# Kernel optimization log

Measured on AMD Instinct MI355X. Metric: run time of the kernel, lower is better.

The kernel has to match this reference:

```python
import jax, jax.numpy as jnp
import numpy as np

D, DFF, H, K = 512, 2048, 8, 31
DK = D // H
EPS = 1e-5


def _ln(x, g, b):
    m = jnp.mean(x, axis=-1, keepdims=True)
    v = jnp.mean((x - m) ** 2, axis=-1, keepdims=True)
    return (x - m) * jax.lax.rsqrt(v + EPS) * g + b


def _ffn(x, w1, b1, w2, b2):
    return jax.nn.silu(x @ w1 + b1) @ w2 + b2


def _rel_shift(x):
    # x: (B, H, T, P) with P = 2T-1
    b, h, q, p = x.shape
    x = jnp.pad(x, ((0, 0), (0, 0), (0, 0), (1, 0)))
    x = x.reshape(b, h, p + 1, q)[:, :, 1:, :]
    return x.reshape(b, h, q, p)


def setup_inputs() -> dict:
    key = jax.random.key(0)
    ks = jax.random.split(key, 32)
    r = lambda i, shape: 0.02 * jax.random.normal(ks[i], shape, dtype=jnp.float32)
    B, T = 4, 1024
    inp = {
        'x': jax.random.normal(ks[0], (B, T, D), dtype=jnp.float32),
        'pos_emb': jax.random.normal(ks[1], (1, 2 * T - 1, D), dtype=jnp.float32),
        # LayerNorms (5)
        'ln1_g': jnp.ones((D,)), 'ln1_b': jnp.zeros((D,)),
        'ln2_g': jnp.ones((D,)), 'ln2_b': jnp.zeros((D,)),
        'ln3_g': jnp.ones((D,)), 'ln3_b': jnp.zeros((D,)),
        'ln4_g': jnp.ones((D,)), 'ln4_b': jnp.zeros((D,)),
        'ln5_g': jnp.ones((D,)), 'ln5_b': jnp.zeros((D,)),
        # FFN1
        'ff1_w1': r(2, (D, DFF)), 'ff1_b1': jnp.zeros((DFF,)),
        'ff1_w2': r(3, (DFF, D)), 'ff1_b2': jnp.zeros((D,)),
        # Attention
        'wq': r(4, (D, D)), 'bq': jnp.zeros((D,)),
        'wk': r(5, (D, D)), 'bk': jnp.zeros((D,)),
        'wv': r(6, (D, D)), 'bv': jnp.zeros((D,)),
        'wp': r(7, (D, D)),
        'wo': r(8, (D, D)), 'bo': jnp.zeros((D,)),
        'pos_u': r(9, (H, DK)), 'pos_v': r(10, (H, DK)),
        # Conv module
        'pw1_w': r(11, (2 * D, D)), 'pw1_b': jnp.zeros((2 * D,)),
        'dw_w': r(12, (D, 1, K)), 'dw_b': jnp.zeros((D,)),
        'bn_g': jnp.ones((D,)), 'bn_b': jnp.zeros((D,)),
        'pw2_w': r(13, (D, D)), 'pw2_b': jnp.zeros((D,)),
        # FFN2
        'ff2_w1': r(14, (D, DFF)), 'ff2_b1': jnp.zeros((DFF,)),
        'ff2_w2': r(15, (DFF, D)), 'ff2_b2': jnp.zeros((D,)),
    }
    return inp


def _attn(x, pos_emb, wq, bq, wk, bk, wv, bv, wp, wo, bo, pos_u, pos_v):
    B, T, _ = x.shape
    q = (x @ wq + bq).reshape(B, T, H, DK).transpose(0, 2, 1, 3)
    k = (x @ wk + bk).reshape(B, T, H, DK).transpose(0, 2, 1, 3)
    v = (x @ wv + bv).reshape(B, T, H, DK).transpose(0, 2, 1, 3)
    P = pos_emb.shape[1]
    p = (pos_emb[0] @ wp).reshape(P, H, DK)  # (P, H, DK)
    ac = jnp.einsum('bhqd,bhkd->bhqk', q + pos_u[:, None, :], k)
    bd = jnp.einsum('bhqd,phd->bhqp', q + pos_v[:, None, :], p)
    bd = _rel_shift(bd)[:, :, :, :T]
    scores = (ac + bd) * (DK ** -0.5)
    attn = jax.nn.softmax(scores, axis=-1)
    out = jnp.einsum('bhqk,bhkd->bhqd', attn, v)
    out = out.transpose(0, 2, 1, 3).reshape(B, T, D)
    return out @ wo + bo


def _conv(x, pw1_w, pw1_b, dw_w, dw_b, bn_g, bn_b, pw2_w, pw2_b):
    y = x.transpose(0, 2, 1)  # (B, D, T)
    y = jnp.einsum('od,bdt->bot', pw1_w, y) + pw1_b[:, None]
    a, g = jnp.split(y, 2, axis=1)
    y = a * jax.nn.sigmoid(g)  # GLU
    pad = (K - 1) // 2
    y = jax.lax.conv_general_dilated(
        y, dw_w, (1,), [(pad, pad)],
        dimension_numbers=('NCW', 'OIW', 'NCW'), feature_group_count=D)
    y = y + dw_b[:, None]
    m = jnp.mean(y, axis=(0, 2), keepdims=True)
    var = jnp.mean((y - m) ** 2, axis=(0, 2), keepdims=True)
    y = (y - m) * jax.lax.rsqrt(var + EPS) * bn_g[:, None] + bn_b[:, None]
    y = jax.nn.silu(y)
    y = jnp.einsum('od,bdt->bot', pw2_w, y) + pw2_b[:, None]
    return y.transpose(0, 2, 1)


def reference(x, pos_emb,
              ln1_g, ln1_b, ff1_w1, ff1_b1, ff1_w2, ff1_b2,
              ln2_g, ln2_b, wq, bq, wk, bk, wv, bv, wp, wo, bo, pos_u, pos_v,
              ln3_g, ln3_b, pw1_w, pw1_b, dw_w, dw_b, bn_g, bn_b, pw2_w, pw2_b,
              ln4_g, ln4_b, ff2_w1, ff2_b1, ff2_w2, ff2_b2,
              ln5_g, ln5_b):
    h = x + 0.5 * _ffn(_ln(x, ln1_g, ln1_b), ff1_w1, ff1_b1, ff1_w2, ff1_b2)
    h = h + _attn(_ln(h, ln2_g, ln2_b), pos_emb, wq, bq, wk, bk, wv, bv, wp, wo, bo, pos_u, pos_v)
    h = h + _conv(_ln(h, ln3_g, ln3_b), pw1_w, pw1_b, dw_w, dw_b, bn_g, bn_b, pw2_w, pw2_b)
    h = h + 0.5 * _ffn(_ln(h, ln4_g, ln4_b), ff2_w1, ff2_b1, ff2_w2, ff2_b2)
    return _ln(h, ln5_g, ln5_b)
```

## Files before the change

kernel.cpp:

```cpp
#include <hip/hip_runtime.h>
#include <math.h>

#define TT   1024
#define BBZ  4
#define DD   512
#define DFF_ 2048
#define HH   8
#define DKK  64
#define NTOK 4096
#define EPSF 1e-5f
#define MB   1048576
#define QSCALE 0.18033688011112042f
#define M0OFF  24.0f

typedef unsigned short u16;
typedef __attribute__((ext_vector_type(8))) short s8v;
typedef __attribute__((ext_vector_type(4))) float f32x4;
typedef __attribute__((ext_vector_type(4))) unsigned short us4;
typedef __attribute__((ext_vector_type(8))) unsigned short us8;

__device__ __forceinline__ float b2f(u16 v){
    union { unsigned int u; float f; } x; x.u = ((unsigned int)v) << 16; return x.f;
}
__device__ __forceinline__ u16 f2b(float f){
    union { float f; unsigned int u; } x; x.f = f;
    unsigned int r = x.u + 0x7fffu + ((x.u >> 16) & 1u);
    return (u16)(r >> 16);
}
__device__ __forceinline__ float sigmoidf_(float x){ return 1.0f/(1.0f+__expf(-x)); }

__device__ __forceinline__ void gld16(const u16* g, u16* l){
    __builtin_amdgcn_global_load_lds(
        (const __attribute__((address_space(1))) unsigned int*)g,
        (__attribute__((address_space(3))) unsigned int*)l, 16, 0, 0);
}

template<int OMODE>
__global__ __launch_bounds__(256) void bgemm128(
    const u16* __restrict__ A, int lda,
    const u16* __restrict__ B, int ldb,
    void* __restrict__ Cv, int ldc, int K,
    const float* __restrict__ bias, int act)
{
    int n0 = blockIdx.x * 128;
    int m0 = blockIdx.y * 128;

    __shared__ u16 As[128*64];
    __shared__ u16 Bs[128*64];

    int t = threadIdx.x;
    int w = t >> 6, l = t & 63;
    int lrow = l >> 3, lslot = l & 7;
    int kswz = (lslot ^ lrow) * 8;
    int wm = w >> 1, wn = w & 1;
    int lr = l & 15, lk = l >> 4;

    f32x4 acc[4][4] = {};

    for (int k0 = 0; k0 < K; k0 += 64){
        #pragma unroll
        for (int it = 0; it < 4; ++it){
            int rb = it*32 + w*8;
            gld16(A + (size_t)(m0 + rb + lrow)*lda + k0 + kswz, &As[rb*64]);
            gld16(B + (size_t)(n0 + rb + lrow)*ldb + k0 + kswz, &Bs[rb*64]);
        }
        __syncthreads();

        s8v af[2][4], bf[2][4];
        #pragma unroll
        for (int kh = 0; kh < 2; ++kh){
            int sl = (kh*4 + lk) ^ (lr & 7);
            #pragma unroll
            for (int mi = 0; mi < 4; ++mi)
                af[kh][mi] = *(const s8v*)&As[(wm*64 + mi*16 + lr)*64 + sl*8];
            #pragma unroll
            for (int ni = 0; ni < 4; ++ni)
                bf[kh][ni] = *(const s8v*)&Bs[(wn*64 + ni*16 + lr)*64 + sl*8];
        }
        #pragma unroll
        for (int kh = 0; kh < 2; ++kh)
            #pragma unroll
            for (int mi = 0; mi < 4; ++mi)
                #pragma unroll
                for (int ni = 0; ni < 4; ++ni)
                    acc[mi][ni] = __builtin_amdgcn_mfma_f32_16x16x32_bf16(
                        af[kh][mi], bf[kh][ni], acc[mi][ni], 0, 0, 0);
        __syncthreads();
    }

    #pragma unroll
    for (int mi = 0; mi < 4; ++mi){
        #pragma unroll
        for (int ni = 0; ni < 4; ++ni){
            int gn = n0 + wn*64 + ni*16 + lr;
            float bval = bias ? bias[gn] : 0.0f;
            #pragma unroll
            for (int r = 0; r < 4; ++r){
                int gm = m0 + wm*64 + mi*16 + lk*4 + r;
                float vv = acc[mi][ni][r] + bval;
                if (act) vv = vv * sigmoidf_(vv);
                if (OMODE == 1){
                    ((u16*)Cv)[(size_t)gm*ldc + gn] = f2b(vv);
                } else {
                    u16* base = (u16*)Cv;
                    size_t idx = (gn < 512)
                        ? ((size_t)gm*512 + gn)*2
                        : ((size_t)gm*512 + (gn-512))*2 + 1;
                    base[idx] = f2b(vv);
                }
            }
        }
    }
}

__global__ __launch_bounds__(256) void qkvp_gemm(
    const u16* __restrict__ xn, const u16* __restrict__ wqT,
    const u16* __restrict__ posb, const u16* __restrict__ wpT,
    u16* __restrict__ qkvbase, u16* __restrict__ pproj,
    const float* __restrict__ bqkv,
    const float* __restrict__ posu, const float* __restrict__ posv)
{
    bool isP = (blockIdx.x >= 12);
    if (isP && blockIdx.y >= 16) return;
    const u16* A = isP ? posb : xn;
    const u16* B = isP ? wpT : wqT;
    int n0 = isP ? (blockIdx.x - 12)*128 : blockIdx.x*128;
    int m0 = blockIdx.y * 128;

    __shared__ u16 As[128*64];
    __shared__ u16 Bs[128*64];

    int t = threadIdx.x;
    int w = t >> 6, l = t & 63;
    int lrow = l >> 3, lslot = l & 7;
    int kswz = (lslot ^ lrow) * 8;
    int wm = w >> 1, wn = w & 1;
    int lr = l & 15, lk = l >> 4;

    f32x4 acc[4][4] = {};

    for (int k0 = 0; k0 < 512; k0 += 64){
        #pragma unroll
        for (int it = 0; it < 4; ++it){
            int rb = it*32 + w*8;
            gld16(A + (size_t)(m0 + rb + lrow)*512 + k0 + kswz, &As[rb*64]);
            gld16(B + (size_t)(n0 + rb + lrow)*512 + k0 + kswz, &Bs[rb*64]);
        }
        __syncthreads();

        s8v af[2][4], bf[2][4];
        #pragma unroll
        for (int kh = 0; kh < 2; ++kh){
            int sl = (kh*4 + lk) ^ (lr & 7);
            #pragma unroll
            for (int mi = 0; mi < 4; ++mi)
                af[kh][mi] = *(const s8v*)&As[(wm*64 + mi*16 + lr)*64 + sl*8];
            #pragma unroll
            for (int ni = 0; ni < 4; ++ni)
                bf[kh][ni] = *(const s8v*)&Bs[(wn*64 + ni*16 + lr)*64 + sl*8];
        }
        #pragma unroll
        for (int kh = 0; kh < 2; ++kh)
            #pragma unroll
            for (int mi = 0; mi < 4; ++mi)
                #pragma unroll
                for (int ni = 0; ni < 4; ++ni)
                    acc[mi][ni] = __builtin_amdgcn_mfma_f32_16x16x32_bf16(
                        af[kh][mi], bf[kh][ni], acc[mi][ni], 0, 0, 0);
        __syncthreads();
    }

    #pragma unroll
    for (int mi = 0; mi < 4; ++mi){
        #pragma unroll
        for (int ni = 0; ni < 4; ++ni){
            int gn = n0 + wn*64 + ni*16 + lr;
            float bval = isP ? 0.0f : bqkv[gn];
            #pragma unroll
            for (int r = 0; r < 4; ++r){
                int gm = m0 + wm*64 + mi*16 + lk*4 + r;
                float vv = acc[mi][ni][r] + bval;
                if (isP){
                    pproj[(size_t)gm*512 + gn] = f2b(vv);
                } else {
                    u16* base = qkvbase;
                    if (gn < 512){
                        size_t idx = (size_t)gm*512 + gn;
                        base[idx]              = f2b((vv + posu[gn])*QSCALE);
                        base[idx + (2u<<20)]   = f2b((vv + posv[gn])*QSCALE);
                    } else if (gn < 1024){
                        base[(4u<<20) + (size_t)gm*512 + (gn-512)] = f2b(vv);
                    } else {
                        int gnp = gn - 1024;
                        int bb = gm >> 10, tt2 = gm & 1023;
                        size_t idx = (((size_t)(bb*8 + (gnp>>6)))*64 + (gnp&63))*1024 + tt2;
                        base[(6u<<20) + idx] = f2b(vv);
                    }
                }
            }
        }
    }
}

__global__ __launch_bounds__(256) void bgemm64(
    const u16* __restrict__ A, int lda,
    const u16* __restrict__ B, int ldb,
    u16* __restrict__ C, int ldc, int K,
    const float* __restrict__ bias, float alpha,
    const u16* __restrict__ resid)
{
    int n0 = blockIdx.x * 64;
    int m0 = blockIdx.y * 64;

    __shared__ u16 As[64*64];
    __shared__ u16 Bs[64*64];

    int t = threadIdx.x;
    int w = t >> 6, l = t & 63;
    int lrow = l >> 3, lslot = l & 7;
    int kswz = (lslot ^ lrow) * 8;
    int wm = w >> 1, wn = w & 1;
    int lr = l & 15, lk = l >> 4;

    f32x4 acc[2][2] = {};

    for (int k0 = 0; k0 < K; k0 += 64){
        #pragma unroll
        for (int it = 0; it < 2; ++it){
            int rb = it*32 + w*8;
            gld16(A + (size_t)(m0 + rb + lrow)*lda + k0 + kswz, &As[rb*64]);
            gld16(B + (size_t)(n0 + rb + lrow)*ldb + k0 + kswz, &Bs[rb*64]);
        }
        __syncthreads();

        s8v af[2][2], bf[2][2];
        #pragma unroll
        for (int kh = 0; kh < 2; ++kh){
            int sl = (kh*4 + lk) ^ (lr & 7);
            #pragma unroll
            for (int mi = 0; mi < 2; ++mi)
                af[kh][mi] = *(const s8v*)&As[(wm*32 + mi*16 + lr)*64 + sl*8];
            #pragma unroll
            for (int ni = 0; ni < 2; ++ni)
                bf[kh][ni] = *(const s8v*)&Bs[(wn*32 + ni*16 + lr)*64 + sl*8];
        }
        #pragma unroll
        for (int kh = 0; kh < 2; ++kh)
            #pragma unroll
            for (int mi = 0; mi < 2; ++mi)
                #pragma unroll
                for (int ni = 0; ni < 2; ++ni)
                    acc[mi][ni] = __builtin_amdgcn_mfma_f32_16x16x32_bf16(
                        af[kh][mi], bf[kh][ni], acc[mi][ni], 0, 0, 0);
        __syncthreads();
    }

    #pragma unroll
    for (int mi = 0; mi < 2; ++mi){
        #pragma unroll
        for (int ni = 0; ni < 2; ++ni){
            int gn = n0 + wn*32 + ni*16 + lr;
            float bval = bias ? bias[gn] : 0.0f;
            #pragma unroll
            for (int r = 0; r < 4; ++r){
                int gm = m0 + wm*32 + mi*16 + lk*4 + r;
                float vv = (acc[mi][ni][r] + bval) * alpha;
                if (resid) vv += b2f(resid[(size_t)gm*ldc + gn]);
                C[(size_t)gm*ldc + gn] = f2b(vv);
            }
        }
    }
}

__global__ __launch_bounds__(256) void bgemm64k(
    const u16* __restrict__ A, int lda,
    const u16* __restrict__ B, int ldb,
    u16* __restrict__ C, int ldc, int K,
    const float* __restrict__ bias, float alpha,
    const float* __restrict__ residF, const u16* __restrict__ residB)
{
    int n0 = blockIdx.x * 64;
    int m0 = blockIdx.y * 64;

    __shared__ u16 As[64*128];
    __shared__ u16 Bs[64*128];

    int t = threadIdx.x;
    int w = t >> 6, l = t & 63;
    int r4 = l >> 4;
    int s16 = l & 15;
    int kswz = (s16 ^ (w*4 + r4)) * 8;
    int wm = w >> 1, wn = w & 1;
    int lr = l & 15, lk = l >> 4;

    f32x4 acc[2][2] = {};

    for (int k0 = 0; k0 < K; k0 += 128){
        #pragma unroll
        for (int cb = 0; cb < 4; ++cb){
            int rowu = cb*16 + w*4;
            gld16(A + (size_t)(m0 + rowu + r4)*lda + k0 + kswz, &As[rowu*128]);
            gld16(B + (size_t)(n0 + rowu + r4)*ldb + k0 + kswz, &Bs[rowu*128]);
        }
        __syncthreads();

        #pragma unroll
        for (int kh = 0; kh < 4; ++kh){
            int sl = ((kh*4 + lk) ^ lr) * 8;
            s8v af[2], bf[2];
            #pragma unroll
            for (int mi = 0; mi < 2; ++mi)
                af[mi] = *(const s8v*)&As[(wm*32 + mi*16 + lr)*128 + sl];
            #pragma unroll
            for (int ni = 0; ni < 2; ++ni)
                bf[ni] = *(const s8v*)&Bs[(wn*32 + ni*16 + lr)*128 + sl];
            #pragma unroll
            for (int mi = 0; mi < 2; ++mi)
                #pragma unroll
                for (int ni = 0; ni < 2; ++ni)
                    acc[mi][ni] = __builtin_amdgcn_mfma_f32_16x16x32_bf16(
                        af[mi], bf[ni], acc[mi][ni], 0, 0, 0);
        }
        __syncthreads();
    }

    #pragma unroll
    for (int mi = 0; mi < 2; ++mi){
        #pragma unroll
        for (int ni = 0; ni < 2; ++ni){
            int gn = n0 + wn*32 + ni*16 + lr;
            float bval = bias ? bias[gn] : 0.0f;
            #pragma unroll
            for (int r = 0; r < 4; ++r){
                int gm = m0 + wm*32 + mi*16 + lk*4 + r;
                float vv = (acc[mi][ni][r] + bval) * alpha;
                size_t idx = (size_t)gm*ldc + gn;
                if (residF) vv += residF[idx];
                if (residB) vv += b2f(residB[idx]);
                C[idx] = f2b(vv);
            }
        }
    }
}

__global__ __launch_bounds__(256) void attn_fused(
    const u16* __restrict__ qub, const u16* __restrict__ qvb,
    const u16* __restrict__ kb,  const u16* __restrict__ vt,
    const u16* __restrict__ pp,  u16* __restrict__ out)
{
    int z = blockIdx.y;
    int b = z >> 3, hh = z & 7;
    int i0 = blockIdx.x * 64;

    __shared__ u16 Kb2[2][64*64];
    __shared__ u16 Vb2[2][64*64];
    __shared__ u16 Pring[3][64*64];
    __shared__ u16 PT[64*64];
    __shared__ float Bandd[4][1024];

    int t = threadIdx.x;
    int w = t >> 6, l = t & 63;
    int lrow = l >> 3, lslot = l & 7;
    int kswz = (lslot ^ lrow) * 8;
    int lr = l & 15, lk = l >> 4;

    #pragma unroll
    for (int it = 0; it < 2; ++it){
        int rb = it*32 + w*8;
        gld16(qub + (size_t)(b*TT + i0 + rb + lrow)*DD + hh*64 + kswz, &PT[rb*64]);
        gld16(qvb + (size_t)(b*TT + i0 + rb + lrow)*DD + hh*64 + kswz,
              (u16*)&Bandd[0][0] + rb*64);
    }
    __syncthreads();
    s8v af_u[2], af_v[2];
    #pragma unroll
    for (int kh = 0; kh < 2; ++kh){
        int sl = (kh*4 + lk) ^ (lr & 7);
        af_u[kh] = *(const s8v*)&PT[(w*16 + lr)*64 + sl*8];
        af_v[kh] = *(const s8v*)((const u16*)&Bandd[0][0] + (w*16 + lr)*64 + sl*8);
    }
    #pragma unroll
    for (int it = 0; it < 2; ++it){
        int rb = it*32 + w*8;
        gld16(kb + (size_t)(b*TT +        rb + lrow)*DD + hh*64 + kswz, &Kb2[0][rb*64]);
        gld16(vt + ((size_t)z*64 + rb + lrow)*TT +                kswz, &Vb2[0][rb*64]);
        gld16(pp + (size_t)(960  - i0 +   rb + lrow)*DD + hh*64 + kswz, &Pring[0][rb*64]);
        gld16(pp + (size_t)(1024 - i0 +   rb + lrow)*DD + hh*64 + kswz, &Pring[1][rb*64]);
    }

    f32x4 o_[4] = {};
    float Lp[4] = {0.f, 0.f, 0.f, 0.f};

    int s0 = 0, s1 = 1, s2 = 2;

    for (int jt = 0; jt < 16; ++jt){
        int cur = jt & 1;
        __syncthreads();

        if (jt < 15){
            #pragma unroll
            for (int it = 0; it < 2; ++it){
                int rb = it*32 + w*8;
                gld16(kb + (size_t)(b*TT + (jt+1)*64 + rb + lrow)*DD + hh*64 + kswz,
                      &Kb2[cur^1][rb*64]);
                gld16(vt + ((size_t)z*64 + rb + lrow)*TT + (jt+1)*64 + kswz,
                      &Vb2[cur^1][rb*64]);
                gld16(pp + (size_t)(960 + (jt+2)*64 - i0 + rb + lrow)*DD + hh*64 + kswz,
                      &Pring[s2][rb*64]);
            }
        }

        f32x4 sac[4] = {};
        f32x4 g[5] = {};
        __builtin_amdgcn_s_setprio(1);
        #pragma unroll
        for (int kh = 0; kh < 2; ++kh){
            int sl = (kh*4 + lk) ^ (lr & 7);
            #pragma unroll
            for (int n = 0; n < 4; ++n){
                s8v bK = *(const s8v*)&Kb2[cur][(n*16 + lr)*64 + sl*8];
                sac[n] = __builtin_amdgcn_mfma_f32_16x16x32_bf16(af_u[kh], bK, sac[n], 0,0,0);
            }
            #pragma unroll
            for (int n = 0; n < 5; ++n){
                int nn = (3 - w) + n;
                const u16* pc = (nn & 4) ? &Pring[s1][0] : &Pring[s0][0];
                s8v bP = *(const s8v*)&pc[(((nn&3)*16) + lr)*64 + sl*8];
                g[n] = __builtin_amdgcn_mfma_f32_16x16x32_bf16(af_v[kh], bP, g[n], 0,0,0);
            }
        }
        __builtin_amdgcn_s_setprio(0);

        #pragma unroll
        for (int n = 0; n < 4; ++n){
            int c = (3 - w + n)*16 + lr;
            int d = (c - 63) & 63;
            int rho = (d >> 2) & 3;
            f32x4 vv;
            if (n == 0){
                #pragma unroll
                for (int r = 0; r < 4; ++r){
                    int iia = w*16 + lk*4 + r;
                    vv[r] = (iia >= 63 - c) ? g[0][r] : g[4][r];
                }
            } else {
                vv = g[n];
            }
            bool sw1 = rho & 1, sw2 = rho & 2;
            float b0 = sw1 ? vv[1] : vv[0];
            float b1 = sw1 ? vv[0] : vv[1];
            float b2 = sw1 ? vv[3] : vv[2];
            float b3 = sw1 ? vv[2] : vv[3];
            f32x4 vvp;
            vvp[0] = sw2 ? b2 : b0;
            vvp[1] = sw2 ? b3 : b1;
            vvp[2] = sw2 ? b0 : b2;
            vvp[3] = sw2 ? b1 : b3;
            *(f32x4*)&Bandd[w][d*16 + ((lk + d) & 3)*4] = vvp;
        }

        float p_[4][4];
        #pragma unroll
        for (int r = 0; r < 4; ++r){
            int ii_l = lk*4 + r;
            float rs = 0.0f;
            #pragma unroll
            for (int n = 0; n < 4; ++n){
                int jj = n*16 + lr;
                int d  = (jj - 16*w - ii_l) & 63;
                float bd = Bandd[w][d*16 + (((ii_l>>2) + d) & 3)*4
                                         + ((ii_l ^ (d>>2)) & 3)];
                float pv = __builtin_amdgcn_exp2f(sac[n][r] + bd - M0OFF);
                p_[n][r] = pv; rs += pv;
            }
            Lp[r] += rs;
        }

        #pragma unroll
        for (int n = 0; n < 4; ++n)
            #pragma unroll
            for (int r = 0; r < 4; ++r){
                int ii  = w*16 + lk*4 + r;
                int col = n*16 + lr;
                int sl  = (col>>3) ^ (ii&7);
                PT[ii*64 + sl*8 + (col&7)] = f2b(p_[n][r]);
            }

        __builtin_amdgcn_s_setprio(1);
        #pragma unroll
        for (int kh = 0; kh < 2; ++kh){
            int sl = (kh*4 + lk) ^ (lr & 7);
            s8v ap = *(const s8v*)&PT[(w*16 + lr)*64 + sl*8];
            #pragma unroll
            for (int n = 0; n < 4; ++n){
                s8v bV = *(const s8v*)&Vb2[cur][(n*16 + lr)*64 + sl*8];
                o_[n] = __builtin_amdgcn_mfma_f32_16x16x32_bf16(ap, bV, o_[n], 0,0,0);
            }
        }
        __builtin_amdgcn_s_setprio(0);
        int tmp = s0; s0 = s1; s1 = s2; s2 = tmp;
    }

    float Lr[4];
    #pragma unroll
    for (int r = 0; r < 4; ++r){
        float Lv = Lp[r];
        #pragma unroll
        for (int msk = 1; msk < 16; msk <<= 1) Lv += __shfl_xor(Lv, msk);
        Lr[r] = 1.0f / Lv;
    }

    #pragma unroll
    for (int n = 0; n < 4; ++n)
        #pragma unroll
        for (int r = 0; r < 4; ++r){
            int i  = i0 + w*16 + lk*4 + r;
            int dk = n*16 + lr;
            out[(size_t)(b*TT + i)*DD + hh*64 + dk] = f2b(o_[n][r] * Lr[r]);
        }
}

template<int IB, int OB>
__global__ __launch_bounds__(256) void ln_kernel(const void* __restrict__ inp,
    const float* __restrict__ g, const float* __restrict__ b, void* __restrict__ outv)
{
    int w = threadIdx.x >> 6, l = threadIdx.x & 63;
    int row = blockIdx.x*4 + w;
    float v[8];
    if (IB){
        us8 xv = ((const us8*)((const u16*)inp + (size_t)row*DD))[l];
        #pragma unroll
        for (int e=0;e<8;e++) v[e] = b2f(xv[e]);
    } else {
        const float4* xr = (const float4*)((const float*)inp + (size_t)row*DD);
        float4 a = xr[2*l], c = xr[2*l+1];
        v[0]=a.x; v[1]=a.y; v[2]=a.z; v[3]=a.w;
        v[4]=c.x; v[5]=c.y; v[6]=c.z; v[7]=c.w;
    }
    float s = 0.f, q = 0.f;
    #pragma unroll
    for (int e=0;e<8;e++){ s += v[e]; q += v[e]*v[e]; }
    #pragma unroll
    for (int msk = 1; msk < 64; msk <<= 1){
        s += __shfl_xor(s, msk);
        q += __shfl_xor(q, msk);
    }
    float mean = s*(1.0f/DD);
    float var  = q*(1.0f/DD) - mean*mean;
    float rinv = rsqrtf(var+EPSF);
    float4 g0 = ((const float4*)g)[2*l], g1 = ((const float4*)g)[2*l+1];
    float4 b0 = ((const float4*)b)[2*l], b1 = ((const float4*)b)[2*l+1];
    float gv[8] = {g0.x,g0.y,g0.z,g0.w,g1.x,g1.y,g1.z,g1.w};
    float bv[8] = {b0.x,b0.y,b0.z,b0.w,b1.x,b1.y,b1.z,b1.w};
    float y[8];
    #pragma unroll
    for (int e=0;e<8;e++) y[e] = (v[e]-mean)*rinv*gv[e] + bv[e];
    if (OB){
        us8 o;
        #pragma unroll
        for (int e=0;e<8;e++) o[e] = f2b(y[e]);
        ((us8*)((u16*)outv + (size_t)row*DD))[l] = o;
    } else {
        float4 o0 = {y[0],y[1],y[2],y[3]};
        float4 o1 = {y[4],y[5],y[6],y[7]};
        float4* op = (float4*)((float*)outv + (size_t)row*DD);
        op[2*l] = o0; op[2*l+1] = o1;
    }
}

struct Prep9 {
    const float* s[9];
    u16* d[9];
    int R[9], C[9];
    int t0[10];
};

__global__ __launch_bounds__(256) void prep_all(Prep9 P,
    const float* __restrict__ pw1_w, const float* __restrict__ pw2_w,
    const float* __restrict__ pos_emb, const float* __restrict__ dw_w,
    const float* __restrict__ bq, const float* __restrict__ bk,
    const float* __restrict__ bv,
    u16* __restrict__ pw1b, u16* __restrict__ pw2b,
    u16* __restrict__ posb, float* __restrict__ wt, float* __restrict__ bqkv)
{
    __shared__ float tile[32][33];
    int bid = blockIdx.x;
    if (bid < 5376){
        int j = 0;
        #pragma unroll
        for (int e=1; e<9; e++) if (bid >= P.t0[e]) j = e;
        int lb = bid - P.t0[j];
        int nx = P.C[j] >> 5;
        int c0 = (lb % nx) << 5;
        int r0 = (lb / nx) << 5;
        const float* in = P.s[j];
        u16* out = P.d[j];
        int R = P.R[j], C = P.C[j];
        int tx = threadIdx.x & 31, ty = threadIdx.x >> 5;
        #pragma unroll
        for (int i=0;i<4;i++){
            int rr = ty + i*8;
            tile[rr][tx] = in[(size_t)(r0+rr)*C + c0+tx];
        }
        __syncthreads();
        #pragma unroll
        for (int i=0;i<4;i++){
            int cc = ty + i*8;
            out[(size_t)(c0+cc)*R + r0+tx] = f2b(tile[tx][cc]);
        }
        return;
    }
    int i = (bid - 5376)*256 + threadIdx.x;
    if (i < 524288) { pw1b[i] = f2b(pw1_w[i]); return; }
    i -= 524288;
    if (i < 262144) { pw2b[i] = f2b(pw2_w[i]); return; }
    i -= 262144;
    if (i < 1048576) { posb[i] = (i < 2047*512) ? f2b(pos_emb[i]) : (u16)0; return; }
    i -= 1048576;
    if (i < 15872) { int kk = i >> 9, d = i & 511; wt[i] = dw_w[d*31+kk]; return; }
    i -= 15872;
    if (i < 1536) bqkv[i] = (i < 512) ? bq[i] : (i < 1024 ? bk[i-512] : bv[i-1024]);
}

__global__ __launch_bounds__(256) void dwconv_kernel(const unsigned int* __restrict__ t2i,
    const float* __restrict__ wt, const float* __restrict__ bias, u16* __restrict__ z,
    float* __restrict__ stats)
{
    int d  = blockIdx.x*256 + threadIdx.x;
    int c  = blockIdx.y;
    int b  = c >> 7;
    int t0 = (c & 127) << 3;
    const unsigned int* pa = t2i + (size_t)b*TT*512 + d;
    float wv[31];
    #pragma unroll
    for (int kk=0;kk<31;kk++) wv[kk] = wt[kk*512 + d];
    float xv[38];
    #pragma unroll
    for (int e=0;e<38;e++){
        int tp = t0 - 15 + e;
        if (tp >= 0 && tp < TT){
            unsigned int pv = pa[(size_t)tp*512];
            float a  = b2f((u16)(pv & 0xffffu));
            float gg = b2f((u16)(pv >> 16));
            xv[e] = a * sigmoidf_(gg);
        } else xv[e] = 0.0f;
    }
    float bsv = bias[d];
    float s = 0.f, q = 0.f;
    #pragma unroll
    for (int j=0;j<8;j++){
        float sum = bsv;
        #pragma unroll
        for (int kk=0;kk<31;kk++) sum = fmaf(xv[j+kk], wv[kk], sum);
        z[(size_t)(b*TT+t0+j)*DD + d] = f2b(sum);
        s += sum; q += sum*sum;
    }
    atomicAdd(&stats[d],       s);
    atomicAdd(&stats[512 + d], q);
}

__global__ __launch_bounds__(256) void bn_apply_kernel(const u16* __restrict__ z,
    const float* __restrict__ stats, const float* __restrict__ g, const float* __restrict__ b,
    u16* __restrict__ out)
{
    int idx = blockIdx.x*256 + threadIdx.x;
    int c = idx & (DD-1);
    float m   = stats[c]*(1.0f/NTOK);
    float var = stats[DD+c]*(1.0f/NTOK) - m*m;
    float vv  = (b2f(z[idx])-m)*rsqrtf(var+EPSF)*g[c] + b[c];
    out[idx]  = f2b(vv*sigmoidf_(vv));
}

extern "C" void kernel_launch(void* const* d_in, const int* in_sizes, int n_in,
                              void* d_out, int out_size, void* d_ws, size_t ws_size,
                              hipStream_t stream)
{
    const float* x       = (const float*)d_in[0];
    const float* pos_emb = (const float*)d_in[1];
    const float* ln1_g=(const float*)d_in[2],  *ln1_b=(const float*)d_in[3];
    const float* ln2_g=(const float*)d_in[4],  *ln2_b=(const float*)d_in[5];
    const float* ln3_g=(const float*)d_in[6],  *ln3_b=(const float*)d_in[7];
    const float* ln4_g=(const float*)d_in[8],  *ln4_b=(const float*)d_in[9];
    const float* ln5_g=(const float*)d_in[10], *ln5_b=(const float*)d_in[11];
    const float* ff1_w1=(const float*)d_in[12], *ff1_b1=(const float*)d_in[13];
    const float* ff1_w2=(const float*)d_in[14], *ff1_b2=(const float*)d_in[15];
    const float* wq=(const float*)d_in[16], *bq=(const float*)d_in[17];
    const float* wk=(const float*)d_in[18], *bk=(const float*)d_in[19];
    const float* wv=(const float*)d_in[20], *bv=(const float*)d_in[21];
    const float* wp=(const float*)d_in[22];
    const float* wo=(const float*)d_in[23], *bo=(const float*)d_in[24];
    const float* pos_u=(const float*)d_in[25], *pos_v=(const float*)d_in[26];
    const float* pw1_w=(const float*)d_in[27], *pw1_b=(const float*)d_in[28];
    const float* dw_w=(const float*)d_in[29],  *dw_b=(const float*)d_in[30];
    const float* bn_g=(const float*)d_in[31],  *bn_b=(const float*)d_in[32];
    const float* pw2_w=(const float*)d_in[33], *pw2_b=(const float*)d_in[34];
    const float* ff2_w1=(const float*)d_in[35], *ff2_b1=(const float*)d_in[36];
    const float* ff2_w2=(const float*)d_in[37], *ff2_b2=(const float*)d_in[38];

    char* W = (char*)d_ws;
    u16*  h     = (u16*) (W);
    u16*  xn    = (u16*) (W + (size_t) 8*MB);
    u16*  wall  = (u16*) (W + (size_t)12*MB);
    u16*  qub   = (u16*) (W + (size_t)28*MB);
    u16*  qvb   = (u16*) (W + (size_t)32*MB);
    u16*  kb    = (u16*) (W + (size_t)36*MB);
    u16*  vt    = (u16*) (W + (size_t)40*MB);
    u16*  pproj = (u16*) (W + (size_t)44*MB);
    char* big   = W + (size_t)48*MB;
    u16*  ffh   = (u16*)big;
    unsigned int* t2i = (unsigned int*)big;
    u16*  t3u   = (u16*)(big + (size_t)8*MB);
    float* stats= (float*)(W + (size_t)112*MB);
    float* wt   = stats + 4096;
    float* bqkv = wt + 15872;

    u16* ff1w1T = wall;
    u16* ff1w2T = wall + 1048576;
    u16* wqT    = wall + 2097152;
    u16* wkT    = wall + 2359296;
    u16* wvT    = wall + 2621440;
    u16* wpT    = wall + 2883584;
    u16* woT    = wall + 3145728;
    u16* ff2w1T = wall + 3407872;
    u16* ff2w2T = wall + 4456448;
    u16* pw1b   = wall + 5505024;
    u16* pw2b   = wall + 6029312;
    u16* posb   = wall + 6291456;

    dim3 blk(256);

    Prep9 P;
    P.s[0]=ff1_w1; P.d[0]=ff1w1T; P.R[0]=512;  P.C[0]=2048;
    P.s[1]=ff1_w2; P.d[1]=ff1w2T; P.R[1]=2048; P.C[1]=512;
    P.s[2]=wq;     P.d[2]=wqT;    P.R[2]=512;  P.C[2]=512;
    P.s[3]=wk;     P.d[3]=wkT;    P.R[3]=512;  P.C[3]=512;
    P.s[4]=wv;     P.d[4]=wvT;    P.R[4]=512;  P.C[4]=512;
    P.s[5]=wp;     P.d[5]=wpT;    P.R[5]=512;  P.C[5]=512;
    P.s[6]=wo;     P.d[6]=woT;    P.R[6]=512;  P.C[6]=512;
    P.s[7]=ff2_w1; P.d[7]=ff2w1T; P.R[7]=512;  P.C[7]=2048;
    P.s[8]=ff2_w2; P.d[8]=ff2w2T; P.R[8]=2048; P.C[8]=512;
    int tc[9] = {1024,1024,256,256,256,256,256,1024,1024};
    P.t0[0]=0; for (int e=0;e<9;e++) P.t0[e+1]=P.t0[e]+tc[e];
    prep_all<<<dim3(5376+7236), blk, 0, stream>>>(P, pw1_w, pw2_w, pos_emb, dw_w,
                                                  bq, bk, bv,
                                                  pw1b, pw2b, posb, wt, bqkv);

    ln_kernel<0,1><<<dim3(NTOK/4), blk, 0, stream>>>(x, ln1_g, ln1_b, xn);
    bgemm128<1><<<dim3(16,32), blk, 0, stream>>>(xn,512, ff1w1T,512,
        ffh,2048, 512, ff1_b1,1);
    bgemm64k<<<dim3(8,64), blk, 0, stream>>>(ffh,2048, ff1w2T,2048,
        h,512, 2048, ff1_b2,0.5f, x, nullptr);

    ln_kernel<1,1><<<dim3(NTOK/4), blk, 0, stream>>>(h, ln2_g, ln2_b, xn);
    qkvp_gemm<<<dim3(16,32), blk, 0, stream>>>(xn, wqT, posb, wpT,
        qub, pproj, bqkv, pos_u, pos_v);

    attn_fused<<<dim3(16,32), blk, 0, stream>>>(qub, qvb, kb, vt, pproj, xn);

    bgemm64<<<dim3(8,64), blk, 0, stream>>>(xn,512, woT,512,
        h,512, 512, bo,1.f, h);

    ln_kernel<1,1><<<dim3(NTOK/4), blk, 0, stream>>>(h, ln3_g, ln3_b, xn);
    bgemm128<6><<<dim3(8,32), blk, 0, stream>>>(xn,512, pw1b,512,
        t2i,1024, 512, pw1_b,0);
    (void)hipMemsetAsync(stats, 0, 4096, stream);
    dwconv_kernel<<<dim3(2,512), blk, 0, stream>>>(t2i, wt, dw_b, t3u, stats);
    bn_apply_kernel<<<dim3(NTOK*DD/256), blk, 0, stream>>>(t3u, stats, bn_g, bn_b, xn);
    bgemm64<<<dim3(8,64), blk, 0, stream>>>(xn,512, pw2b,512,
        h,512, 512, pw2_b,1.f, h);

    ln_kernel<1,1><<<dim3(NTOK/4), blk, 0, stream>>>(h, ln4_g, ln4_b, xn);
    bgemm128<1><<<dim3(16,32), blk, 0, stream>>>(xn,512, ff2w1T,512,
        ffh,2048, 512, ff2_b1,1);
    bgemm64k<<<dim3(8,64), blk, 0, stream>>>(ffh,2048, ff2w2T,2048,
        h,512, 2048, ff2_b2,0.5f, nullptr, h);

    ln_kernel<1,0><<<dim3(NTOK/4), blk, 0, stream>>>(h, ln5_g, ln5_b, (float*)d_out);
}
```

Before: 265.5 us.

## Fuse LN1 and stats clear into prep kernel; remap attention blocks per XCD

The first LayerNorm and the BatchNorm stats zeroing are folded into the prep_all kernel as extra block ranges, which removes one kernel launch and one memset from the sequence. The attention grid becomes 1-D and is remapped so that all blocks for a given head are assigned to the same XCD, aiming for better L2 reuse of that head's K, V and position data. The fused LayerNorm computes variance in a single pass (E[x²]−mean²), which is slightly less numerically robust than a two-pass version. Both additions depend on hardcoded block offsets inside prep_all.

```diff
diff --git a/kernel.cpp b/kernel.cpp
--- a/kernel.cpp
+++ b/kernel.cpp
@@ -348,9 +348,14 @@
     const u16* __restrict__ kb,  const u16* __restrict__ vt,
     const u16* __restrict__ pp,  u16* __restrict__ out)
 {
-    int z = blockIdx.y;
-    int b = z >> 3, hh = z & 7;
-    int i0 = blockIdx.x * 64;
+    int s   = blockIdx.x;
+    int xcd = s & 7;
+    int k9  = s >> 3;
+    int zhi = k9 >> 4;
+    int xx  = k9 & 15;
+    int z   = (zhi << 3) | xcd;
+    int b = zhi, hh = xcd;
+    int i0 = xx * 64;
 
     __shared__ u16 Kb2[2][64*64];
     __shared__ u16 Vb2[2][64*64];
@@ -581,7 +586,10 @@
     const float* __restrict__ bq, const float* __restrict__ bk,
     const float* __restrict__ bv,
     u16* __restrict__ pw1b, u16* __restrict__ pw2b,
-    u16* __restrict__ posb, float* __restrict__ wt, float* __restrict__ bqkv)
+    u16* __restrict__ posb, float* __restrict__ wt, float* __restrict__ bqkv,
+    const float* __restrict__ x, const float* __restrict__ ln1_g,
+    const float* __restrict__ ln1_b, u16* __restrict__ xn,
+    float* __restrict__ stats)
 {
     __shared__ float tile[32][33];
     int bid = blockIdx.x;
@@ -608,6 +616,38 @@
             int cc = ty + i*8;
             out[(size_t)(c0+cc)*R + r0+tx] = f2b(tile[tx][cc]);
         }
+        return;
+    }
+    if (bid >= 12612 && bid < 13636){
+        int w = threadIdx.x >> 6, l = threadIdx.x & 63;
+        int row = (bid - 12612)*4 + w;
+        const float4* xr = (const float4*)(x + (size_t)row*DD);
+        float4 a = xr[2*l], c = xr[2*l+1];
+        float v[8] = {a.x,a.y,a.z,a.w,c.x,c.y,c.z,c.w};
+        float s = 0.f, q = 0.f;
+        #pragma unroll
+        for (int e=0;e<8;e++){ s += v[e]; q += v[e]*v[e]; }
+        #pragma unroll
+        for (int msk = 1; msk < 64; msk <<= 1){
+            s += __shfl_xor(s, msk);
+            q += __shfl_xor(q, msk);
+        }
+        float mean = s*(1.0f/DD);
+        float var  = q*(1.0f/DD) - mean*mean;
+        float rinv = rsqrtf(var+EPSF);
+        float4 g0 = ((const float4*)ln1_g)[2*l], g1 = ((const float4*)ln1_g)[2*l+1];
+        float4 b0 = ((const float4*)ln1_b)[2*l], b1 = ((const float4*)ln1_b)[2*l+1];
+        float gv[8] = {g0.x,g0.y,g0.z,g0.w,g1.x,g1.y,g1.z,g1.w};
+        float bv[8] = {b0.x,b0.y,b0.z,b0.w,b1.x,b1.y,b1.z,b1.w};
+        us8 o;
+        #pragma unroll
+        for (int e=0;e<8;e++) o[e] = f2b((v[e]-mean)*rinv*gv[e] + bv[e]);
+        ((us8*)(xn + (size_t)row*DD))[l] = o;
+        return;
+    }
+    if (bid >= 13636){
+        int i = threadIdx.x;
+        stats[i] = 0.0f; stats[256+i] = 0.0f; stats[512+i] = 0.0f; stats[768+i] = 0.0f;
         return;
     }
     int i = (bid - 5376)*256 + threadIdx.x;
@@ -741,11 +781,11 @@
     P.s[8]=ff2_w2; P.d[8]=ff2w2T; P.R[8]=2048; P.C[8]=512;
     int tc[9] = {1024,1024,256,256,256,256,256,1024,1024};
     P.t0[0]=0; for (int e=0;e<9;e++) P.t0[e+1]=P.t0[e]+tc[e];
-    prep_all<<<dim3(5376+7236), blk, 0, stream>>>(P, pw1_w, pw2_w, pos_emb, dw_w,
-                                                  bq, bk, bv,
-                                                  pw1b, pw2b, posb, wt, bqkv);
-
-    ln_kernel<0,1><<<dim3(NTOK/4), blk, 0, stream>>>(x, ln1_g, ln1_b, xn);
+    prep_all<<<dim3(13637), blk, 0, stream>>>(P, pw1_w, pw2_w, pos_emb, dw_w,
+                                              bq, bk, bv,
+                                              pw1b, pw2b, posb, wt, bqkv,
+                                              x, ln1_g, ln1_b, xn, stats);
+
     bgemm128<1><<<dim3(16,32), blk, 0, stream>>>(xn,512, ff1w1T,512,
         ffh,2048, 512, ff1_b1,1);
     bgemm64k<<<dim3(8,64), blk, 0, stream>>>(ffh,2048, ff1w2T,2048,
@@ -755,7 +795,7 @@
     qkvp_gemm<<<dim3(16,32), blk, 0, stream>>>(xn, wqT, posb, wpT,
         qub, pproj, bqkv, pos_u, pos_v);
 
-    attn_fused<<<dim3(16,32), blk, 0, stream>>>(qub, qvb, kb, vt, pproj, xn);
+    attn_fused<<<dim3(512), blk, 0, stream>>>(qub, qvb, kb, vt, pproj, xn);
 
     bgemm64<<<dim3(8,64), blk, 0, stream>>>(xn,512, woT,512,
         h,512, 512, bo,1.f, h);
@@ -763,7 +803,6 @@
     ln_kernel<1,1><<<dim3(NTOK/4), blk, 0, stream>>>(h, ln3_g, ln3_b, xn);
     bgemm128<6><<<dim3(8,32), blk, 0, stream>>>(xn,512, pw1b,512,
         t2i,1024, 512, pw1_b,0);
-    (void)hipMemsetAsync(stats, 0, 4096, stream);
     dwconv_kernel<<<dim3(2,512), blk, 0, stream>>>(t2i, wt, dw_b, t3u, stats);
     bn_apply_kernel<<<dim3(NTOK*DD/256), blk, 0, stream>>>(t3u, stats, bn_g, bn_b, xn);
     bgemm64<<<dim3(8,64), blk, 0, stream>>>(xn,512, pw2b,512,
```

After: 261.4 us. No clear change (-1.5%).
